# Kernel optimization log

Measured on AMD Instinct MI355X. Metric: run time of the kernel, lower is better.

The kernel has to match this reference:

```python
import jax, jax.numpy as jnp
import numpy as np

B, N1, N2 = 16, 196, 196
C1, C2, H, O = 768, 768, 512, 128


def setup_inputs() -> dict:
    key = jax.random.key(0)
    k1, k2, kw1, kw2, kwp, kbp = jax.random.split(key, 6)
    x1 = jax.random.normal(k1, (B, N1, C1), dtype=jnp.float32)
    x2 = jax.random.normal(k2, (B, N2, C2), dtype=jnp.float32)
    # kaiming-uniform-ish init scale
    W1 = jax.random.uniform(kw1, (C1, H), dtype=jnp.float32, minval=-1, maxval=1) * np.sqrt(3.0 / C1)
    W2 = jax.random.uniform(kw2, (C2, H), dtype=jnp.float32, minval=-1, maxval=1) * np.sqrt(3.0 / C2)
    Wp = jax.random.uniform(kwp, (H, O), dtype=jnp.float32, minval=-1, maxval=1) * np.sqrt(3.0 / H)
    bp = jax.random.uniform(kbp, (O,), dtype=jnp.float32, minval=-1, maxval=1) * (1.0 / np.sqrt(H))
    return {"x1": x1, "x2": x2, "W1": W1, "W2": W2, "Wp": Wp, "bp": bp}


def reference(x1, x2, W1, W2, Wp, bp):
    # x1: [B,N1,C1], x2: [B,N2,C2]
    h1 = jax.nn.relu(jnp.einsum('bnc,ch->bnh', x1, W1))  # [B,N1,H]
    h2 = jax.nn.relu(jnp.einsum('bmc,ch->bmh', x2, W2))  # [B,N2,H]
    # Original: ((h1[:,:,None,:] * h2[:,None,:,:]) @ Wp + bp).sum(dim=(1,2)).
    # Mathematically identical fused form: sum_{i,j} h1[b,i,h]*h2[b,j,h]
    #   = (sum_i h1)[b,h] * (sum_j h2)[b,h]; bias accumulates N1*N2 times.
    s = h1.sum(axis=1) * h2.sum(axis=1)                   # [B,H]
    return jnp.einsum('bh,ho->bo', s, Wp) + bp * (N1 * N2)
```

## Files before the change

### kernel.cpp

```cpp
#include <hip/hip_runtime.h>
#include <hip/hip_bf16.h>


#define NB 16
#define NROW 196
#define KC_ 768
#define HH 512
#define OO 128

using short4v = __attribute__((ext_vector_type(4))) short;
using short8 = __attribute__((ext_vector_type(8))) short;
using f32x16 = __attribute__((ext_vector_type(16))) float;

__device__ __forceinline__ short2 pk2bf(float a, float b) {
    __hip_bfloat162 h = __float22bfloat162_rn(make_float2(a, b));
    union { __hip_bfloat162 h; short2 s; } u; u.h = h;
    return u.s;
}

__global__ __launch_bounds__(256)
void w_tile(const float* __restrict__ W1, const float* __restrict__ W2,
            unsigned short* __restrict__ Wt) {
    const int bb = blockIdx.x;
    const int branch = bb / 48;
    const int rem = bb % 48;
    const int ht = rem / 12;
    const int kc = rem % 12;
    const float* __restrict__ W = branch ? W2 : W1;
    unsigned short* __restrict__ out = Wt + (size_t)bb * 8192;
    const int t = threadIdx.x;
#pragma unroll
    for (int i = 0; i < 4; ++i) {
        const int u = i * 256 + t;
        const int p = u >> 7, col = u & 127;
        const float* src = W + (kc * 64 + p * 8) * HH + ht * 128 + col;
        float f[8];
#pragma unroll
        for (int j = 0; j < 8; ++j) f[j] = src[j * HH];
        short8 v; short2 s;
#pragma unroll
        for (int j = 0; j < 4; ++j) {
            s = pk2bf(f[2 * j], f[2 * j + 1]); v[2 * j] = s.x; v[2 * j + 1] = s.y;
        }
        *(short8*)(out + u * 8) = v;
    }
}

__global__ __launch_bounds__(512, 1)
void gemm_relu_rowsum(const float* __restrict__ x1, const float* __restrict__ x2,
                      const unsigned short* __restrict__ Wt,
                      float* __restrict__ sbuf) {
    __shared__ unsigned short Alds[2][8 * 129 * 8];
    __shared__ unsigned short Blds[2][8 * 129 * 8];
    __shared__ float psum[16 * 32];

    const int bid = blockIdx.x;
    const int p  = bid & 31;
    const int tt = bid >> 5;
    const int branch = p >> 4;
    const int b      = p & 15;
    const int ht = tt >> 1;
    const int mh = tt & 1;

    const float* __restrict__ x = branch ? x2 : x1;
    const unsigned short* __restrict__ Wtb = Wt + (size_t)((branch * 4 + ht) * 12) * 8192;

    const int t   = threadIdx.x;
    const int l16 = t & 15;
    const int rg  = t >> 4;
    const float* xbase = x + (b * NROW + mh * 128) * KC_ + l16 * 4;

    const int bp0 = t >> 7,          bc0 = t & 127;
    const int bp1 = (t + 512) >> 7,  bc1 = t & 127;

    float4 av[4];
    short8 bva, bvb;

    auto load_stage = [&](int kc) {
#pragma unroll
        for (int r = 0; r < 4; ++r) {
            const int row = rg + 32 * r;
            if (mh * 128 + row < NROW)
                av[r] = *(const float4*)(xbase + row * KC_ + kc * 64);
            else
                av[r] = make_float4(0.f, 0.f, 0.f, 0.f);
        }
        const unsigned short* wc = Wtb + kc * 8192;
        bva = *(const short8*)(wc + bp0 * 1024 + bc0 * 8);
        bvb = *(const short8*)(wc + bp1 * 1024 + bc1 * 8);
    };

    auto write_stage = [&](int buf) {
#pragma unroll
        for (int r = 0; r < 4; ++r) {
            short4v sv; short2 s;
            s = pk2bf(av[r].x, av[r].y); sv[0] = s.x; sv[1] = s.y;
            s = pk2bf(av[r].z, av[r].w); sv[2] = s.x; sv[3] = s.y;
            const int row = rg + 32 * r;
            *(short4v*)&Alds[buf][((l16 >> 1) * 129 + row) * 8 + (l16 & 1) * 4] = sv;
        }
        *(short8*)&Blds[buf][(bp0 * 129 + bc0) * 8] = bva;
        *(short8*)&Blds[buf][(bp1 * 129 + bc1) * 8] = bvb;
    };

    const int w  = t >> 6;
    const int l  = t & 63;
    const int m  = l & 31;
    const int q  = l >> 5;
    const int sp = w & 1;
    const int mp = w >> 1;
    const int aoff = (mp * 32 + m) * 8;
    const int boff = (sp * 64 + m) * 8;

    f32x16 acc0 = {}, acc1 = {};

    load_stage(0);
    write_stage(0);
    load_stage(1);
    __syncthreads();

#pragma unroll 1
    for (int kc = 0; kc < 12; ++kc) {
        const int pb = kc & 1;
#pragma unroll
        for (int ks = 0; ks < 4; ++ks) {
            const int base = (ks * 2 + q) * 129 * 8;
            short8 af = *(const short8*)&Alds[pb][base + aoff];
            short8 b0 = *(const short8*)&Blds[pb][base + boff];
            short8 b1 = *(const short8*)&Blds[pb][base + boff + 256];
            acc0 = __builtin_amdgcn_mfma_f32_32x32x16_bf16(af, b0, acc0, 0, 0, 0);
            acc1 = __builtin_amdgcn_mfma_f32_32x32x16_bf16(af, b1, acc1, 0, 0, 0);
        }
        if (kc < 11) write_stage(1 - pb);
        if (kc < 10) load_stage(kc + 2);
        __syncthreads();
    }

    float cs0 = 0.f, cs1 = 0.f;
#pragma unroll
    for (int r = 0; r < 16; ++r) {
        cs0 += fmaxf(acc0[r], 0.f);
        cs1 += fmaxf(acc1[r], 0.f);
    }
    cs0 += __shfl_xor(cs0, 32);
    cs1 += __shfl_xor(cs1, 32);
    if (l < 32) {
        psum[((sp * 2 + 0) * 4 + mp) * 32 + l] = cs0;
        psum[((sp * 2 + 1) * 4 + mp) * 32 + l] = cs1;
    }
    __syncthreads();
    if (t < 128) {
        const int ct = t >> 5;
        const int cl = t & 31;
        float v = 0.f;
#pragma unroll
        for (int mp2 = 0; mp2 < 4; ++mp2)
            v += psum[(ct * 4 + mp2) * 32 + cl];
        sbuf[((branch * 2 + mh) * NB + b) * HH + ht * 128 + t] = v;
    }
}

__global__ __launch_bounds__(512)
void proj_kernel(const float* __restrict__ sbuf, const float* __restrict__ Wp,
                 const float* __restrict__ bp, float* __restrict__ out) {
    __shared__ float spl[HH];
    __shared__ float red[4][OO];
    const int b = blockIdx.x, t = threadIdx.x;
    {
        const float s1 = sbuf[(0 * NB + b) * HH + t] + sbuf[(1 * NB + b) * HH + t];
        const float s2 = sbuf[(2 * NB + b) * HH + t] + sbuf[(3 * NB + b) * HH + t];
        spl[t] = s1 * s2;
    }
    __syncthreads();
    const int to = t & 127, hq = t >> 7;
    float acc = 0.f;
#pragma unroll 8
    for (int h = hq * 128; h < hq * 128 + 128; ++h)
        acc += spl[h] * Wp[h * OO + to];
    red[hq][to] = acc;
    __syncthreads();
    if (t < OO)
        out[b * OO + t] = red[0][t] + red[1][t] + red[2][t] + red[3][t]
                        + bp[t] * 38416.0f;
}

extern "C" void kernel_launch(void* const* d_in, const int* in_sizes, int n_in,
                              void* d_out, int out_size, void* d_ws, size_t ws_size,
                              hipStream_t stream) {
    const float* x1 = (const float*)d_in[0];
    const float* x2 = (const float*)d_in[1];
    const float* W1 = (const float*)d_in[2];
    const float* W2 = (const float*)d_in[3];
    const float* Wp = (const float*)d_in[4];
    const float* bp = (const float*)d_in[5];
    float* sbuf = (float*)d_ws;
    unsigned short* Wt = (unsigned short*)((char*)d_ws + 131072);

    w_tile<<<96, 256, 0, stream>>>(W1, W2, Wt);
    gemm_relu_rowsum<<<256, 512, 0, stream>>>(x1, x2, Wt, sbuf);
    proj_kernel<<<NB, 512, 0, stream>>>(sbuf, Wp, bp, (float*)d_out);
}
```

Before: 94.07 us.

## Pre-convert activations to tiled bf16 in a pretile kernel before GEMM

Activation conversion from fp32 to bf16 moves out of the GEMM main loop into a combined pretile kernel, which also tiles the weights and writes x into a contiguous per-stage bf16 layout in workspace. The GEMM then streams both operands with plain contiguous 16-byte loads and LDS stores, dropping the padded 129-stride layout and the in-loop packing. This cuts fp32 reads in the GEMM (each x tile was read 4 times, once per ht block) but adds an extra round trip of the bf16 x buffer through global memory. The pretile x part runs on only 64 blocks with a serial kc loop, and removing the padding may add LDS bank conflicts.

```diff
diff --git a/kernel.cpp b/kernel.cpp
--- a/kernel.cpp
+++ b/kernel.cpp
@@ -8,7 +8,6 @@
 #define HH 512
 #define OO 128
 
-using short4v = __attribute__((ext_vector_type(4))) short;
 using short8 = __attribute__((ext_vector_type(8))) short;
 using f32x16 = __attribute__((ext_vector_type(16))) float;
 
@@ -19,39 +18,83 @@
 }
 
 __global__ __launch_bounds__(256)
-void w_tile(const float* __restrict__ W1, const float* __restrict__ W2,
-            unsigned short* __restrict__ Wt) {
-    const int bb = blockIdx.x;
-    const int branch = bb / 48;
-    const int rem = bb % 48;
-    const int ht = rem / 12;
-    const int kc = rem % 12;
-    const float* __restrict__ W = branch ? W2 : W1;
-    unsigned short* __restrict__ out = Wt + (size_t)bb * 8192;
+void pretile(const float* __restrict__ x1, const float* __restrict__ x2,
+             const float* __restrict__ W1, const float* __restrict__ W2,
+             unsigned short* __restrict__ Wt, unsigned short* __restrict__ Xt) {
     const int t = threadIdx.x;
-#pragma unroll
-    for (int i = 0; i < 4; ++i) {
-        const int u = i * 256 + t;
-        const int p = u >> 7, col = u & 127;
-        const float* src = W + (kc * 64 + p * 8) * HH + ht * 128 + col;
-        float f[8];
-#pragma unroll
-        for (int j = 0; j < 8; ++j) f[j] = src[j * HH];
-        short8 v; short2 s;
-#pragma unroll
-        for (int j = 0; j < 4; ++j) {
-            s = pk2bf(f[2 * j], f[2 * j + 1]); v[2 * j] = s.x; v[2 * j + 1] = s.y;
+    if (blockIdx.x < 96) {
+        const int bb = blockIdx.x;
+        const int branch = bb / 48;
+        const int rem = bb % 48;
+        const int ht = rem / 12;
+        const int kc = rem % 12;
+        const float* __restrict__ W = branch ? W2 : W1;
+        unsigned short* __restrict__ out = Wt + (size_t)bb * 8192;
+#pragma unroll
+        for (int i = 0; i < 4; ++i) {
+            const int u = i * 256 + t;
+            const int p = u >> 7, col = u & 127;
+            const float* src = W + (kc * 64 + p * 8) * HH + ht * 128 + col;
+            float f[8];
+#pragma unroll
+            for (int j = 0; j < 8; ++j) f[j] = src[j * HH];
+            short8 v; short2 s;
+#pragma unroll
+            for (int j = 0; j < 4; ++j) {
+                s = pk2bf(f[2 * j], f[2 * j + 1]); v[2 * j] = s.x; v[2 * j + 1] = s.y;
+            }
+            *(short8*)(out + u * 8) = v;
         }
-        *(short8*)(out + u * 8) = v;
+    } else {
+        const int xb = blockIdx.x - 96;
+        const int branch = xb >> 5;
+        const int b  = (xb & 31) >> 1;
+        const int mh = xb & 1;
+        const float* __restrict__ x = branch ? x2 : x1;
+        unsigned short* __restrict__ outb =
+            Xt + (size_t)(((branch * 16 + b) * 2 + mh) * 12) * 8192;
+#pragma unroll 1
+        for (int kc = 0; kc < 12; ++kc) {
+            unsigned short* __restrict__ out = outb + kc * 8192;
+#pragma unroll
+            for (int h = 0; h < 2; ++h) {
+                const int v = h * 256 + t;
+                const int row = v >> 2, g = v & 3;
+                const int r_abs = mh * 128 + row;
+                float4 f0, f1;
+                if (r_abs < NROW) {
+                    const float* src = x + ((size_t)(b * NROW + r_abs)) * KC_ + kc * 64 + g * 16;
+                    f0 = *(const float4*)(src);
+                    f1 = *(const float4*)(src + 4);
+                    float4 f2 = *(const float4*)(src + 8);
+                    float4 f3 = *(const float4*)(src + 12);
+                    short8 v0, v1; short2 s;
+                    s = pk2bf(f0.x, f0.y); v0[0] = s.x; v0[1] = s.y;
+                    s = pk2bf(f0.z, f0.w); v0[2] = s.x; v0[3] = s.y;
+                    s = pk2bf(f1.x, f1.y); v0[4] = s.x; v0[5] = s.y;
+                    s = pk2bf(f1.z, f1.w); v0[6] = s.x; v0[7] = s.y;
+                    s = pk2bf(f2.x, f2.y); v1[0] = s.x; v1[1] = s.y;
+                    s = pk2bf(f2.z, f2.w); v1[2] = s.x; v1[3] = s.y;
+                    s = pk2bf(f3.x, f3.y); v1[4] = s.x; v1[5] = s.y;
+                    s = pk2bf(f3.z, f3.w); v1[6] = s.x; v1[7] = s.y;
+                    *(short8*)(out + ((2 * g + 0) * 128 + row) * 8) = v0;
+                    *(short8*)(out + ((2 * g + 1) * 128 + row) * 8) = v1;
+                } else {
+                    short8 z = {};
+                    *(short8*)(out + ((2 * g + 0) * 128 + row) * 8) = z;
+                    *(short8*)(out + ((2 * g + 1) * 128 + row) * 8) = z;
+                }
+            }
+        }
     }
 }
 
 __global__ __launch_bounds__(512, 1)
-void gemm_relu_rowsum(const float* __restrict__ x1, const float* __restrict__ x2,
+void gemm_relu_rowsum(const unsigned short* __restrict__ Xt,
                       const unsigned short* __restrict__ Wt,
                       float* __restrict__ sbuf) {
-    __shared__ unsigned short Alds[2][8 * 129 * 8];
-    __shared__ unsigned short Blds[2][8 * 129 * 8];
+    __shared__ unsigned short Alds[2][8192];
+    __shared__ unsigned short Blds[2][8192];
     __shared__ float psum[16 * 32];
 
     const int bid = blockIdx.x;
@@ -62,45 +105,27 @@
     const int ht = tt >> 1;
     const int mh = tt & 1;
 
-    const float* __restrict__ x = branch ? x2 : x1;
-    const unsigned short* __restrict__ Wtb = Wt + (size_t)((branch * 4 + ht) * 12) * 8192;
-
-    const int t   = threadIdx.x;
-    const int l16 = t & 15;
-    const int rg  = t >> 4;
-    const float* xbase = x + (b * NROW + mh * 128) * KC_ + l16 * 4;
-
-    const int bp0 = t >> 7,          bc0 = t & 127;
-    const int bp1 = (t + 512) >> 7,  bc1 = t & 127;
-
-    float4 av[4];
-    short8 bva, bvb;
-
+    const unsigned short* __restrict__ Xc =
+        Xt + (size_t)(((branch * 16 + b) * 2 + mh) * 12) * 8192;
+    const unsigned short* __restrict__ Wc =
+        Wt + (size_t)((branch * 4 + ht) * 12) * 8192;
+
+    const int t = threadIdx.x;
+
+    short8 a0r, a1r, b0r, b1r;
     auto load_stage = [&](int kc) {
-#pragma unroll
-        for (int r = 0; r < 4; ++r) {
-            const int row = rg + 32 * r;
-            if (mh * 128 + row < NROW)
-                av[r] = *(const float4*)(xbase + row * KC_ + kc * 64);
-            else
-                av[r] = make_float4(0.f, 0.f, 0.f, 0.f);
-        }
-        const unsigned short* wc = Wtb + kc * 8192;
-        bva = *(const short8*)(wc + bp0 * 1024 + bc0 * 8);
-        bvb = *(const short8*)(wc + bp1 * 1024 + bc1 * 8);
+        const unsigned short* xc = Xc + kc * 8192;
+        const unsigned short* wc = Wc + kc * 8192;
+        a0r = *(const short8*)(xc + t * 8);
+        a1r = *(const short8*)(xc + (t + 512) * 8);
+        b0r = *(const short8*)(wc + t * 8);
+        b1r = *(const short8*)(wc + (t + 512) * 8);
     };
-
     auto write_stage = [&](int buf) {
-#pragma unroll
-        for (int r = 0; r < 4; ++r) {
-            short4v sv; short2 s;
-            s = pk2bf(av[r].x, av[r].y); sv[0] = s.x; sv[1] = s.y;
-            s = pk2bf(av[r].z, av[r].w); sv[2] = s.x; sv[3] = s.y;
-            const int row = rg + 32 * r;
-            *(short4v*)&Alds[buf][((l16 >> 1) * 129 + row) * 8 + (l16 & 1) * 4] = sv;
-        }
-        *(short8*)&Blds[buf][(bp0 * 129 + bc0) * 8] = bva;
-        *(short8*)&Blds[buf][(bp1 * 129 + bc1) * 8] = bvb;
+        *(short8*)&Alds[buf][t * 8]          = a0r;
+        *(short8*)&Alds[buf][(t + 512) * 8]  = a1r;
+        *(short8*)&Blds[buf][t * 8]          = b0r;
+        *(short8*)&Blds[buf][(t + 512) * 8]  = b1r;
     };
 
     const int w  = t >> 6;
@@ -124,7 +149,7 @@
         const int pb = kc & 1;
 #pragma unroll
         for (int ks = 0; ks < 4; ++ks) {
-            const int base = (ks * 2 + q) * 129 * 8;
+            const int base = (ks * 2 + q) * 1024;
             short8 af = *(const short8*)&Alds[pb][base + aoff];
             short8 b0 = *(const short8*)&Blds[pb][base + boff];
             short8 b1 = *(const short8*)&Blds[pb][base + boff + 256];
@@ -194,9 +219,10 @@
     const float* Wp = (const float*)d_in[4];
     const float* bp = (const float*)d_in[5];
     float* sbuf = (float*)d_ws;
-    unsigned short* Wt = (unsigned short*)((char*)d_ws + 131072);
-
-    w_tile<<<96, 256, 0, stream>>>(W1, W2, Wt);
-    gemm_relu_rowsum<<<256, 512, 0, stream>>>(x1, x2, Wt, sbuf);
+    unsigned short* Wt = (unsigned short*)((char*)d_ws + (131072));
+    unsigned short* Xt = (unsigned short*)((char*)d_ws + (131072 + 1572864));
+
+    pretile<<<160, 256, 0, stream>>>(x1, x2, W1, W2, Wt, Xt);
+    gemm_relu_rowsum<<<256, 512, 0, stream>>>(Xt, Wt, sbuf);
     proj_kernel<<<NB, 512, 0, stream>>>(sbuf, Wp, bp, (float*)d_out);
 }
```

Result: slower. 101.4 us (+7.8%).

## Split GEMM row tiles into quarters with 256-thread blocks and unpadded LDS

Applied to the files above, without the earlier changes.

Each GEMM block now covers 64 rows instead of 128 and runs 256 threads, so the grid doubles to 512 blocks with two blocks per CU. Partial row sums for four row quarters go into a larger sbuf, which proj_kernel now sums. The LDS layout drops the 129-stride padding, and each thread loads a contiguous 16-float chunk of one row, stored as two 16-byte LDS writes. The aim is better CU occupancy and less padding waste. In exchange, every W tile is re-read twice as often and the unpadded LDS reads may hit bank conflicts.

```diff
diff --git a/kernel.cpp b/kernel.cpp
--- a/kernel.cpp
+++ b/kernel.cpp
@@ -8,7 +8,6 @@
 #define HH 512
 #define OO 128
 
-using short4v = __attribute__((ext_vector_type(4))) short;
 using short8 = __attribute__((ext_vector_type(8))) short;
 using f32x16 = __attribute__((ext_vector_type(16))) float;
 
@@ -21,6 +20,7 @@
 __global__ __launch_bounds__(256)
 void w_tile(const float* __restrict__ W1, const float* __restrict__ W2,
             unsigned short* __restrict__ Wt) {
+    const int t = threadIdx.x;
     const int bb = blockIdx.x;
     const int branch = bb / 48;
     const int rem = bb % 48;
@@ -28,7 +28,6 @@
     const int kc = rem % 12;
     const float* __restrict__ W = branch ? W2 : W1;
     unsigned short* __restrict__ out = Wt + (size_t)bb * 8192;
-    const int t = threadIdx.x;
 #pragma unroll
     for (int i = 0; i < 4; ++i) {
         const int u = i * 256 + t;
@@ -46,61 +45,65 @@
     }
 }
 
-__global__ __launch_bounds__(512, 1)
+__global__ __launch_bounds__(256, 2)
 void gemm_relu_rowsum(const float* __restrict__ x1, const float* __restrict__ x2,
                       const unsigned short* __restrict__ Wt,
                       float* __restrict__ sbuf) {
-    __shared__ unsigned short Alds[2][8 * 129 * 8];
-    __shared__ unsigned short Blds[2][8 * 129 * 8];
-    __shared__ float psum[16 * 32];
+    __shared__ unsigned short Alds[2][8 * 64 * 8];
+    __shared__ unsigned short Blds[2][8 * 128 * 8];
+    __shared__ float psum[8 * 32];
 
     const int bid = blockIdx.x;
     const int p  = bid & 31;
     const int tt = bid >> 5;
     const int branch = p >> 4;
     const int b      = p & 15;
-    const int ht = tt >> 1;
-    const int mh = tt & 1;
+    const int ht = tt >> 2;
+    const int mq = tt & 3;
 
     const float* __restrict__ x = branch ? x2 : x1;
     const unsigned short* __restrict__ Wtb = Wt + (size_t)((branch * 4 + ht) * 12) * 8192;
 
-    const int t   = threadIdx.x;
-    const int l16 = t & 15;
-    const int rg  = t >> 4;
-    const float* xbase = x + (b * NROW + mh * 128) * KC_ + l16 * 4;
-
-    const int bp0 = t >> 7,          bc0 = t & 127;
-    const int bp1 = (t + 512) >> 7,  bc1 = t & 127;
+    const int t    = threadIdx.x;
+    const int row  = t >> 2;
+    const int slot = t & 3;
+    const int r_abs = mq * 64 + row;
+    const bool valid = r_abs < NROW;
+    const float* xrow = x + (b * NROW + (valid ? r_abs : 0)) * KC_ + slot * 16;
 
     float4 av[4];
-    short8 bva, bvb;
+    short8 bv[4];
 
     auto load_stage = [&](int kc) {
-#pragma unroll
-        for (int r = 0; r < 4; ++r) {
-            const int row = rg + 32 * r;
-            if (mh * 128 + row < NROW)
-                av[r] = *(const float4*)(xbase + row * KC_ + kc * 64);
-            else
-                av[r] = make_float4(0.f, 0.f, 0.f, 0.f);
+        if (valid) {
+#pragma unroll
+            for (int i = 0; i < 4; ++i)
+                av[i] = *(const float4*)(xrow + kc * 64 + 4 * i);
+        } else {
+#pragma unroll
+            for (int i = 0; i < 4; ++i) av[i] = make_float4(0.f, 0.f, 0.f, 0.f);
         }
         const unsigned short* wc = Wtb + kc * 8192;
-        bva = *(const short8*)(wc + bp0 * 1024 + bc0 * 8);
-        bvb = *(const short8*)(wc + bp1 * 1024 + bc1 * 8);
+#pragma unroll
+        for (int i = 0; i < 4; ++i)
+            bv[i] = *(const short8*)(wc + (t + 256 * i) * 8);
     };
 
     auto write_stage = [&](int buf) {
-#pragma unroll
-        for (int r = 0; r < 4; ++r) {
-            short4v sv; short2 s;
-            s = pk2bf(av[r].x, av[r].y); sv[0] = s.x; sv[1] = s.y;
-            s = pk2bf(av[r].z, av[r].w); sv[2] = s.x; sv[3] = s.y;
-            const int row = rg + 32 * r;
-            *(short4v*)&Alds[buf][((l16 >> 1) * 129 + row) * 8 + (l16 & 1) * 4] = sv;
-        }
-        *(short8*)&Blds[buf][(bp0 * 129 + bc0) * 8] = bva;
-        *(short8*)&Blds[buf][(bp1 * 129 + bc1) * 8] = bvb;
+        short8 v0, v1; short2 s;
+        s = pk2bf(av[0].x, av[0].y); v0[0] = s.x; v0[1] = s.y;
+        s = pk2bf(av[0].z, av[0].w); v0[2] = s.x; v0[3] = s.y;
+        s = pk2bf(av[1].x, av[1].y); v0[4] = s.x; v0[5] = s.y;
+        s = pk2bf(av[1].z, av[1].w); v0[6] = s.x; v0[7] = s.y;
+        s = pk2bf(av[2].x, av[2].y); v1[0] = s.x; v1[1] = s.y;
+        s = pk2bf(av[2].z, av[2].w); v1[2] = s.x; v1[3] = s.y;
+        s = pk2bf(av[3].x, av[3].y); v1[4] = s.x; v1[5] = s.y;
+        s = pk2bf(av[3].z, av[3].w); v1[6] = s.x; v1[7] = s.y;
+        *(short8*)&Alds[buf][((slot * 2 + 0) * 64 + row) * 8] = v0;
+        *(short8*)&Alds[buf][((slot * 2 + 1) * 64 + row) * 8] = v1;
+#pragma unroll
+        for (int i = 0; i < 4; ++i)
+            *(short8*)&Blds[buf][(t + 256 * i) * 8] = bv[i];
     };
 
     const int w  = t >> 6;
@@ -124,10 +127,10 @@
         const int pb = kc & 1;
 #pragma unroll
         for (int ks = 0; ks < 4; ++ks) {
-            const int base = (ks * 2 + q) * 129 * 8;
-            short8 af = *(const short8*)&Alds[pb][base + aoff];
-            short8 b0 = *(const short8*)&Blds[pb][base + boff];
-            short8 b1 = *(const short8*)&Blds[pb][base + boff + 256];
+            const int kp = ks * 2 + q;
+            short8 af = *(const short8*)&Alds[pb][kp * 512 + aoff];
+            short8 b0 = *(const short8*)&Blds[pb][kp * 1024 + boff];
+            short8 b1 = *(const short8*)&Blds[pb][kp * 1024 + boff + 256];
             acc0 = __builtin_amdgcn_mfma_f32_32x32x16_bf16(af, b0, acc0, 0, 0, 0);
             acc1 = __builtin_amdgcn_mfma_f32_32x32x16_bf16(af, b1, acc1, 0, 0, 0);
         }
@@ -145,18 +148,15 @@
     cs0 += __shfl_xor(cs0, 32);
     cs1 += __shfl_xor(cs1, 32);
     if (l < 32) {
-        psum[((sp * 2 + 0) * 4 + mp) * 32 + l] = cs0;
-        psum[((sp * 2 + 1) * 4 + mp) * 32 + l] = cs1;
+        psum[((sp * 2 + 0) * 2 + mp) * 32 + l] = cs0;
+        psum[((sp * 2 + 1) * 2 + mp) * 32 + l] = cs1;
     }
     __syncthreads();
     if (t < 128) {
         const int ct = t >> 5;
         const int cl = t & 31;
-        float v = 0.f;
-#pragma unroll
-        for (int mp2 = 0; mp2 < 4; ++mp2)
-            v += psum[(ct * 4 + mp2) * 32 + cl];
-        sbuf[((branch * 2 + mh) * NB + b) * HH + ht * 128 + t] = v;
+        const float v = psum[(ct * 2 + 0) * 32 + cl] + psum[(ct * 2 + 1) * 32 + cl];
+        sbuf[((branch * 4 + mq) * NB + b) * HH + ht * 128 + t] = v;
     }
 }
 
@@ -167,8 +167,12 @@
     __shared__ float red[4][OO];
     const int b = blockIdx.x, t = threadIdx.x;
     {
-        const float s1 = sbuf[(0 * NB + b) * HH + t] + sbuf[(1 * NB + b) * HH + t];
-        const float s2 = sbuf[(2 * NB + b) * HH + t] + sbuf[(3 * NB + b) * HH + t];
+        float s1 = 0.f, s2 = 0.f;
+#pragma unroll
+        for (int i = 0; i < 4; ++i) {
+            s1 += sbuf[((0 + i) * NB + b) * HH + t];
+            s2 += sbuf[((4 + i) * NB + b) * HH + t];
+        }
         spl[t] = s1 * s2;
     }
     __syncthreads();
@@ -194,9 +198,9 @@
     const float* Wp = (const float*)d_in[4];
     const float* bp = (const float*)d_in[5];
     float* sbuf = (float*)d_ws;
-    unsigned short* Wt = (unsigned short*)((char*)d_ws + 131072);
+    unsigned short* Wt = (unsigned short*)((char*)d_ws + 262144);
 
     w_tile<<<96, 256, 0, stream>>>(W1, W2, Wt);
-    gemm_relu_rowsum<<<256, 512, 0, stream>>>(x1, x2, Wt, sbuf);
+    gemm_relu_rowsum<<<512, 256, 0, stream>>>(x1, x2, Wt, sbuf);
     proj_kernel<<<NB, 512, 0, stream>>>(sbuf, Wp, bp, (float*)d_out);
 }
```

Result: no change. 95.12 us (+1.1%).
